# Kernel tuning notes

Measured on AMD Instinct MI355X. Metric: run time of the kernel, lower is better.

Reference implementation:

```python
import jax, jax.numpy as jnp
import numpy as np


def gru_cell(x, h, Wih, Whh, bih, bhh):
    # torch GRU cell, gate order r, z, n
    gi = x @ Wih.T + bih
    gh = h @ Whh.T + bhh
    ir, iz, inn = jnp.split(gi, 3, axis=-1)
    hr, hz, hn = jnp.split(gh, 3, axis=-1)
    r = jax.nn.sigmoid(ir + hr)
    z = jax.nn.sigmoid(iz + hz)
    n = jnp.tanh(inn + r * hn)
    return (1.0 - z) * n + z * h


def setup_inputs() -> dict:
    key = jax.random.key(0)
    ks = jax.random.split(key, 24)
    S, T, B, E, H, V = 64, 64, 32, 512, 1024, 32000
    sc_e = 1.0 / np.sqrt(E)
    sc_h = 1.0 / np.sqrt(H)

    def rn(i, shape, sc):
        return jax.random.normal(ks[i], shape, jnp.float32) * sc

    return {
        "src": jax.random.randint(ks[0], (S, B), 0, V),
        "trg": jax.random.randint(ks[1], (T, B), 0, V),
        "emb": rn(2, (V, E), 0.02),
        # encoder forward-direction GRU
        "Wih_f": rn(3, (3 * H, E), sc_e), "Whh_f": rn(4, (3 * H, H), sc_h),
        "bih_f": rn(5, (3 * H,), sc_h), "bhh_f": rn(6, (3 * H,), sc_h),
        # encoder backward-direction GRU
        "Wih_b": rn(7, (3 * H, E), sc_e), "Whh_b": rn(8, (3 * H, H), sc_h),
        "bih_b": rn(9, (3 * H,), sc_h), "bhh_b": rn(10, (3 * H,), sc_h),
        # attention: Linear(2H -> H) and scoring vector v
        "Wa": rn(11, (H, 2 * H), sc_h), "ba": rn(12, (H,), sc_h),
        "v": rn(13, (H,), sc_h),
        # decoder GRU: input is [embedded(E); context(H)]
        "Wih_d": rn(14, (3 * H, E + H), sc_h), "Whh_d": rn(15, (3 * H, H), sc_h),
        "bih_d": rn(16, (3 * H,), sc_h), "bhh_d": rn(17, (3 * H,), sc_h),
        # output head Linear(2H -> V)
        "Wout": rn(18, (V, 2 * H), sc_h), "bout": rn(19, (V,), sc_h),
    }


def reference(src, trg, emb, Wih_f, Whh_f, bih_f, bhh_f, Wih_b, Whh_b, bih_b, bhh_b,
              Wa, ba, v, Wih_d, Whh_d, bih_d, bhh_d, Wout, bout):
    S, B = src.shape
    H = Whh_f.shape[1]

    # ---- encoder: bidirectional GRU, fwd+bwd output halves summed ----
    src_emb = emb[src]  # [S, B, E]
    h0 = jnp.zeros((B, H), src_emb.dtype)

    def step_f(h, x):
        h2 = gru_cell(x, h, Wih_f, Whh_f, bih_f, bhh_f)
        return h2, h2

    def step_b(h, x):
        h2 = gru_cell(x, h, Wih_b, Whh_b, bih_b, bhh_b)
        return h2, h2

    h_fwd, out_f = jax.lax.scan(step_f, h0, src_emb)
    _, out_b_rev = jax.lax.scan(step_b, h0, src_emb[::-1])
    enc_out = out_f + out_b_rev[::-1]          # [S, B, H]
    enc_bt = enc_out.transpose(1, 0, 2)        # [B, S, H]

    # ---- decoder with teacher forcing (ratio fixed to 1.0) ----
    dec_tokens = jnp.concatenate([src[-1:], trg[:-1]], axis=0)  # [T, B]
    dec_emb = emb[dec_tokens]                                   # [T, B, E]

    def dec_step(h, e_t):
        # Bahdanau attention: relu(Linear([h; enc])) scored by v
        hrep = jnp.broadcast_to(h[:, None, :], enc_bt.shape)    # [B, S, H]
        energy = jax.nn.relu(jnp.concatenate([hrep, enc_bt], -1) @ Wa.T + ba)
        scores = energy @ v                                     # [B, S]
        a = jax.nn.softmax(scores, axis=1)
        ctx = jnp.einsum('bs,bsh->bh', a, enc_bt)               # [B, H]
        rnn_in = jnp.concatenate([e_t, ctx], axis=-1)           # [B, E+H]
        h_new = gru_cell(rnn_in, h, Wih_d, Whh_d, bih_d, bhh_d)
        logits = jnp.concatenate([h_new, ctx], -1) @ Wout.T + bout  # [B, V]
        return h_new, logits

    _, outputs = jax.lax.scan(dec_step, h_fwd, dec_emb)  # [T, B, V]
    return outputs
```

## Files before the change

### kernel.cpp

```cpp
#include <hip/hip_runtime.h>
#include <hip/hip_bf16.h>

#define S_ 64
#define T_ 64
#define B_ 32
#define E_ 512
#define H_ 1024
#define V_ 32000
#define H3 3072
#define H2 2048
#define EH 1536

typedef unsigned short u16;
typedef unsigned int u32;
typedef unsigned long long u64;
typedef __attribute__((ext_vector_type(8))) short bf16x8;
typedef __attribute__((ext_vector_type(4))) float f32x4;

#define MFMA3(ACC, AH_, AL_, BH_, BL_)                                              \
    ACC = __builtin_amdgcn_mfma_f32_16x16x32_bf16(AL_, BH_, ACC, 0, 0, 0);          \
    ACC = __builtin_amdgcn_mfma_f32_16x16x32_bf16(AH_, BL_, ACC, 0, 0, 0);          \
    ACC = __builtin_amdgcn_mfma_f32_16x16x32_bf16(AH_, BH_, ACC, 0, 0, 0);

__device__ __forceinline__ void splitf(float x, u16& h, u16& l) {
    u32 xb = __float_as_uint(x);
    u32 hb = (xb + 0x7FFFu + ((xb >> 16) & 1u)) & 0xFFFF0000u;
    h = (u16)(hb >> 16);
    float lf = x - __uint_as_float(hb);
    u32 lb = __float_as_uint(lf);
    l = (u16)((lb + 0x7FFFu + ((lb >> 16) & 1u)) >> 16);
}

__device__ __forceinline__ float bf2f(u16 v) { return __uint_as_float(((u32)v) << 16); }

__device__ __forceinline__ void load_lds16(const void* g, void* l) {
    __builtin_amdgcn_global_load_lds((const __attribute__((address_space(1))) u32*)g,
                                     (__attribute__((address_space(3))) u32*)l, 16, 0, 0);
}

__device__ __forceinline__ bf16x8 ld_sys16(const u16* p) {
    union { bf16x8 v; u64 q[2]; } u;
    const u64* q = (const u64*)p;
    u.q[0] = __hip_atomic_load(q,     __ATOMIC_RELAXED, __HIP_MEMORY_SCOPE_SYSTEM);
    u.q[1] = __hip_atomic_load(q + 1, __ATOMIC_RELAXED, __HIP_MEMORY_SCOPE_SYSTEM);
    return u.v;
}
__device__ __forceinline__ float ld_sysf(const float* p) {
    return __hip_atomic_load(p, __ATOMIC_RELAXED, __HIP_MEMORY_SCOPE_SYSTEM);
}
__device__ __forceinline__ void st_sysf(float* p, float v) {
    __hip_atomic_store(p, v, __ATOMIC_RELAXED, __HIP_MEMORY_SCOPE_SYSTEM);
}
__device__ __forceinline__ void st_sysu16(u16* p, u16 v) {
    __hip_atomic_store(p, v, __ATOMIC_RELAXED, __HIP_MEMORY_SCOPE_SYSTEM);
}

__device__ __forceinline__ void gbar(int* cnt, int* flag, int nblk, int blk, int& gen) {
    __syncthreads();
    if (threadIdx.x == 0) {
        gen += 1;
        asm volatile("s_waitcnt vmcnt(0)" ::: "memory");
        __hip_atomic_fetch_add(&cnt[(blk & 7) << 5], 1, __ATOMIC_RELAXED,
                               __HIP_MEMORY_SCOPE_SYSTEM);
        if (blk == 0) {
            const int target = nblk * gen;
            for (;;) {
                int sum = 0;
#pragma unroll
                for (int j = 0; j < 8; ++j)
                    sum += __hip_atomic_load(&cnt[j << 5], __ATOMIC_RELAXED,
                                             __HIP_MEMORY_SCOPE_SYSTEM);
                if (sum >= target) break;
                __builtin_amdgcn_s_sleep(2);
            }
#pragma unroll
            for (int j = 0; j < 8; ++j)
                __hip_atomic_store(&flag[j << 5], gen, __ATOMIC_RELAXED,
                                   __HIP_MEMORY_SCOPE_SYSTEM);
        } else {
            while (__hip_atomic_load(&flag[(blk & 7) << 5], __ATOMIC_RELAXED,
                                     __HIP_MEMORY_SCOPE_SYSTEM) < gen)
                __builtin_amdgcn_s_sleep(2);
        }
    }
    __syncthreads();
}

__device__ __forceinline__ void gbar_grp(int* cnt, int grp, int n, int& gen) {
    __syncthreads();
    if (threadIdx.x == 0) {
        gen += 1;
        asm volatile("s_waitcnt vmcnt(0)" ::: "memory");
        __hip_atomic_fetch_add(&cnt[grp << 5], 1, __ATOMIC_RELAXED,
                               __HIP_MEMORY_SCOPE_SYSTEM);
        const int target = n * gen;
        while (__hip_atomic_load(&cnt[grp << 5], __ATOMIC_RELAXED,
                                 __HIP_MEMORY_SCOPE_SYSTEM) < target)
            __builtin_amdgcn_s_sleep(1);
    }
    __syncthreads();
}

__global__ void k_embed_src_split(const int* __restrict__ src, const float* __restrict__ emb,
                                  u16* __restrict__ hi, u16* __restrict__ lo) {
    int row = blockIdx.x;
    int tok = src[row];
    int c = threadIdx.x * 4;
    float4 v = *reinterpret_cast<const float4*>(emb + (size_t)tok * E_ + c);
    ushort4 h, l;
    splitf(v.x, h.x, l.x); splitf(v.y, h.y, l.y);
    splitf(v.z, h.z, l.z); splitf(v.w, h.w, l.w);
    *reinterpret_cast<ushort4*>(hi + (size_t)row * E_ + c) = h;
    *reinterpret_cast<ushort4*>(lo + (size_t)row * E_ + c) = l;
}

__global__ void k_embed_dec_split(const int* __restrict__ src, const int* __restrict__ trg,
                                  const float* __restrict__ emb,
                                  u16* __restrict__ hi, u16* __restrict__ lo) {
    int row = blockIdx.x;
    int t = row >> 5, b = row & 31;
    int tok = (t == 0) ? src[(S_ - 1) * B_ + b] : trg[(t - 1) * B_ + b];
    int c = threadIdx.x * 4;
    float4 v = *reinterpret_cast<const float4*>(emb + (size_t)tok * E_ + c);
    ushort4 h, l;
    splitf(v.x, h.x, l.x); splitf(v.y, h.y, l.y);
    splitf(v.z, h.z, l.z); splitf(v.w, h.w, l.w);
    *reinterpret_cast<ushort4*>(hi + (size_t)row * E_ + c) = h;
    *reinterpret_cast<ushort4*>(lo + (size_t)row * E_ + c) = l;
}

__global__ __launch_bounds__(256) void k_split(const float* __restrict__ in, int ld, int cols4,
                                               u16* __restrict__ hi, u16* __restrict__ lo) {
    int c4 = blockIdx.x * 256 + threadIdx.x;
    if (c4 >= cols4) return;
    size_t r = blockIdx.y;
    float4 v = *reinterpret_cast<const float4*>(in + r * ld + (size_t)c4 * 4);
    ushort4 h, l;
    splitf(v.x, h.x, l.x); splitf(v.y, h.y, l.y);
    splitf(v.z, h.z, l.z); splitf(v.w, h.w, l.w);
    size_t o = (r * cols4 + c4) * 4;
    *reinterpret_cast<ushort4*>(hi + o) = h;
    *reinterpret_cast<ushort4*>(lo + o) = l;
}

__global__ __launch_bounds__(256) void k_split_sum_enc(
    const float* __restrict__ ef, const float* __restrict__ eb, float* __restrict__ es,
    u16* __restrict__ hi, u16* __restrict__ lo) {
    size_t r = blockIdx.y;
    int c4 = threadIdx.x * 4;
    float4 va = *reinterpret_cast<const float4*>(ef + r * H_ + c4);
    float4 vb = *reinterpret_cast<const float4*>(eb + r * H_ + c4);
    float4 v; v.x = va.x + vb.x; v.y = va.y + vb.y; v.z = va.z + vb.z; v.w = va.w + vb.w;
    *reinterpret_cast<float4*>(es + r * H_ + c4) = v;
    ushort4 h, l;
    splitf(v.x, h.x, l.x); splitf(v.y, h.y, l.y);
    splitf(v.z, h.z, l.z); splitf(v.w, h.w, l.w);
    *reinterpret_cast<ushort4*>(hi + r * H_ + c4) = h;
    *reinterpret_cast<ushort4*>(lo + r * H_ + c4) = l;
}

__global__ void k_wsplit_perm(const float* __restrict__ src, int ld, int coff,
                              u16* __restrict__ hi, u16* __restrict__ lo) {
    int r = blockIdx.x;
    int i = r / 3, g = r - i * 3;
    const float* p = src + (size_t)(g * H_ + i) * ld + coff;
    int c = threadIdx.x * 4;
    float4 v = *reinterpret_cast<const float4*>(p + c);
    ushort4 h, l;
    splitf(v.x, h.x, l.x); splitf(v.y, h.y, l.y);
    splitf(v.z, h.z, l.z); splitf(v.w, h.w, l.w);
    *reinterpret_cast<ushort4*>(hi + (size_t)r * H_ + c) = h;
    *reinterpret_cast<ushort4*>(lo + (size_t)r * H_ + c) = l;
}

__global__ __launch_bounds__(256, 2) void k_gemm_mfma3(
    const u16* __restrict__ Ah, const u16* __restrict__ Al,
    const u16* __restrict__ Bh, const u16* __restrict__ Bl,
    const float* __restrict__ bias, float* __restrict__ C,
    int ldc, int K)
{
    __shared__ u16 ls[4][128 * 32];
    const int tid = threadIdx.x;
    const int lane = tid & 63, w = tid >> 6;
    const int wr = w >> 1, wc = w & 1;
    const size_t m0 = (size_t)blockIdx.x * 128, n0 = (size_t)blockIdx.y * 128;

    const int c0 = (w * 2) * 64 + lane;
    const int r0 = c0 >> 2, kc0 = (c0 & 3) << 3;
    const size_t rstep = (size_t)16 * K;
    const u16* gAh = Ah + (m0 + r0) * K + kc0;
    const u16* gAl = Al + (m0 + r0) * K + kc0;
    const u16* gBh = Bh + (n0 + r0) * K + kc0;
    const u16* gBl = Bl + (n0 + r0) * K + kc0;
    const int lo0 = c0 * 8;

    const int frow = lane & 15, fk = (lane >> 4) << 3;
    const int offA = (wr * 64 + frow) * 32 + fk;
    const int offB = (wc * 64 + frow) * 32 + fk;

    f32x4 acc[4][4] = {};

    for (int k0 = 0; k0 < K; k0 += 32) {
        load_lds16(gAh + k0, &ls[0][lo0]);
        load_lds16(gAh + rstep + k0, &ls[0][lo0 + 512]);
        load_lds16(gAl + k0, &ls[1][lo0]);
        load_lds16(gAl + rstep + k0, &ls[1][lo0 + 512]);
        load_lds16(gBh + k0, &ls[2][lo0]);
        load_lds16(gBh + rstep + k0, &ls[2][lo0 + 512]);
        load_lds16(gBl + k0, &ls[3][lo0]);
        load_lds16(gBl + rstep + k0, &ls[3][lo0 + 512]);
        __syncthreads();

        bf16x8 fAh[4], fAl[4], fBh[4], fBl[4];
#pragma unroll
        for (int m = 0; m < 4; ++m) {
            fAh[m] = *reinterpret_cast<const bf16x8*>(&ls[0][offA + m * 512]);
            fAl[m] = *reinterpret_cast<const bf16x8*>(&ls[1][offA + m * 512]);
        }
#pragma unroll
        for (int n = 0; n < 4; ++n) {
            fBh[n] = *reinterpret_cast<const bf16x8*>(&ls[2][offB + n * 512]);
            fBl[n] = *reinterpret_cast<const bf16x8*>(&ls[3][offB + n * 512]);
        }
#pragma unroll
        for (int m = 0; m < 4; ++m)
#pragma unroll
            for (int n = 0; n < 4; ++n) {
                MFMA3(acc[m][n], fAh[m], fAl[m], fBh[n], fBl[n]);
            }
        __syncthreads();
    }

    const int crow0 = wr * 64 + ((lane >> 4) << 2);
    const int ccol0 = wc * 64 + (lane & 15);
#pragma unroll
    for (int n = 0; n < 4; ++n) {
        const size_t col = n0 + ccol0 + n * 16;
        const float bv = bias ? bias[col] : 0.f;
#pragma unroll
        for (int m = 0; m < 4; ++m)
#pragma unroll
            for (int r = 0; r < 4; ++r)
                C[(m0 + crow0 + m * 16 + r) * (size_t)ldc + col] = acc[m][n][r] + bv;
    }
}

__global__ __launch_bounds__(256, 2) void k_gemm_n2f(
    const u16* __restrict__ Ah, const u16* __restrict__ Al,
    const float* __restrict__ Bf,
    const float* __restrict__ bias, float* __restrict__ C,
    int ldc, int K)
{
    __shared__ u16 lsA[2][128 * 32];
    __shared__ u16 lsBh[256 * 32];
    __shared__ u16 lsBl[256 * 32];
    const int tid = threadIdx.x;
    const int lane = tid & 63, w = tid >> 6;
    const int wr = w >> 1, wc = w & 1;
    const size_t m0 = (size_t)blockIdx.x * 128, n0 = (size_t)blockIdx.y * 256;

    const int frow = lane & 15, fk = (lane >> 4) << 3;
    const int offA = (wr * 64 + frow) * 32 + fk;
    const int offB = (wc * 128 + frow) * 32 + fk;

    f32x4 acc[4][8] = {};

    for (int k0 = 0; k0 < K; k0 += 32) {
#pragma unroll
        for (int q = 0; q < 4; ++q) {
            const int chunk = (w + q * 4) * 64 + lane;
            const int local = chunk & 511;
            const u16* A = (chunk < 512) ? Ah : Al;
            load_lds16(A + (m0 + (local >> 2)) * K + k0 + ((local & 3) << 3),
                       &lsA[chunk >> 9][local * 8]);
        }
#pragma unroll
        for (int q = 0; q < 4; ++q) {
            const int c = tid + q * 256;
            const int row = c >> 2, k8 = (c & 3) << 3;
            const float* src = Bf + (size_t)(n0 + row) * K + k0 + k8;
            float4 v0 = *reinterpret_cast<const float4*>(src);
            float4 v1 = *reinterpret_cast<const float4*>(src + 4);
            union { ushort4 s[2]; bf16x8 v; } hh, ll;
            splitf(v0.x, hh.s[0].x, ll.s[0].x); splitf(v0.y, hh.s[0].y, ll.s[0].y);
            splitf(v0.z, hh.s[0].z, ll.s[0].z); splitf(v0.w, hh.s[0].w, ll.s[0].w);
            splitf(v1.x, hh.s[1].x, ll.s[1].x); splitf(v1.y, hh.s[1].y, ll.s[1].y);
            splitf(v1.z, hh.s[1].z, ll.s[1].z); splitf(v1.w, hh.s[1].w, ll.s[1].w);
            *reinterpret_cast<bf16x8*>(&lsBh[row * 32 + k8]) = hh.v;
            *reinterpret_cast<bf16x8*>(&lsBl[row * 32 + k8]) = ll.v;
        }
        __syncthreads();

        bf16x8 fAh[4], fAl[4];
#pragma unroll
        for (int m = 0; m < 4; ++m) {
            fAh[m] = *reinterpret_cast<const bf16x8*>(&lsA[0][offA + m * 512]);
            fAl[m] = *reinterpret_cast<const bf16x8*>(&lsA[1][offA + m * 512]);
        }
#pragma unroll
        for (int n = 0; n < 8; ++n) {
            bf16x8 fBh = *reinterpret_cast<const bf16x8*>(&lsBh[offB + n * 512]);
            bf16x8 fBl = *reinterpret_cast<const bf16x8*>(&lsBl[offB + n * 512]);
#pragma unroll
            for (int m = 0; m < 4; ++m) {
                MFMA3(acc[m][n], fAh[m], fAl[m], fBh, fBl);
            }
        }
        __syncthreads();
    }

    const int crow0 = wr * 64 + ((lane >> 4) << 2);
    const int ccol0 = wc * 128 + (lane & 15);
#pragma unroll
    for (int n = 0; n < 8; ++n) {
        const size_t col = n0 + ccol0 + n * 16;
        const float bv = bias ? bias[col] : 0.f;
#pragma unroll
        for (int m = 0; m < 4; ++m)
#pragma unroll
            for (int r = 0; r < 4; ++r)
                C[(m0 + crow0 + m * 16 + r) * (size_t)ldc + col] = acc[m][n][r] + bv;
    }
}

__global__ __launch_bounds__(256) void k_enc_persist(
    const u16* __restrict__ whhf_h, const u16* __restrict__ whhf_l,
    const u16* __restrict__ whhb_h, const u16* __restrict__ whhb_l,
    const float* __restrict__ gi_f, const float* __restrict__ gi_b,
    const float* __restrict__ bhh_f, const float* __restrict__ bhh_b,
    u16* __restrict__ hfH0, u16* __restrict__ hfL0,
    u16* __restrict__ hfH1, u16* __restrict__ hfL1,
    u16* __restrict__ hbH0, u16* __restrict__ hbL0,
    u16* __restrict__ hbH1, u16* __restrict__ hbL1,
    float* __restrict__ enc_f, float* __restrict__ enc_b,
    int* __restrict__ cnt, int* __restrict__ flag)
{
    __shared__ __align__(16) char smem[145792];
    u16* lAh  = (u16*)smem;
    u16* lAl  = (u16*)(smem + 65536);
    float* ex0 = (float*)(smem + 131072);
    float* ex1 = (float*)(smem + 137408);
    float* hloc = (float*)(smem + 143744);

    const int blk = blockIdx.x, tid = threadIdx.x;
    const int lane = tid & 63, w = tid >> 6;
    const int dir = blk >> 6, c = blk & 63;
    const int i0 = c * 16;
    const u16* WH = (dir ? whhb_h : whhf_h) + (size_t)c * 48 * 1024;
    const u16* WL = (dir ? whhb_l : whhf_l) + (size_t)c * 48 * 1024;
    const float* gi = dir ? gi_b : gi_f;
    const float* bhh = dir ? bhh_b : bhh_f;
    float* encd = dir ? enc_b : enc_f;
    int* cntd  = cnt + dir * 256;
    int* flagd = flag + dir * 256;
    int gen = 0;

    for (int q = tid; q < 512; q += 256) hloc[q] = 0.f;

    const int frow = lane & 15, fk8 = (lane >> 4) << 3;
    const int cb = lane & 15, rb0 = (lane >> 4) << 2;

    for (int t = 0; t < 64; ++t) {
        const int a = t & 1;
        const u16* rH = dir ? (a ? hbH1 : hbH0) : (a ? hfH1 : hfH0);
        const u16* rL = dir ? (a ? hbL1 : hbL0) : (a ? hfL1 : hfL0);
        u16* oH = dir ? (a ? hbH0 : hbH1) : (a ? hfH0 : hfH1);
        u16* oL = dir ? (a ? hbL0 : hbL1) : (a ? hfL0 : hfL1);
        const int s = dir ? 63 - t : t;

#pragma unroll
        for (int ch0 = 0; ch0 < 4096; ch0 += 256) {
            int ch = ch0 + tid;
            int r = ch >> 7, kc = (ch & 127) << 3;
            int sw = kc ^ ((r & 7) << 3);
            *(bf16x8*)&lAh[r * 1024 + sw] = ld_sys16(&rH[r * 1024 + kc]);
            *(bf16x8*)&lAl[r * 1024 + sw] = ld_sys16(&rL[r * 1024 + kc]);
        }
        __syncthreads();

#pragma unroll
        for (int jj = 0; jj < 3; ++jj) {
            const int j = w * 3 + jj;
            const int m = j & 1;
            const int n = (j >> 1) % 3;
            const int kh = j / 6;
            const int arow = m * 16 + frow;
            const int asw = (arow & 7) << 3;
            const u16* gBh = WH + (size_t)(n * 16 + frow) * 1024;
            const u16* gBl = WL + (size_t)(n * 16 + frow) * 1024;
            f32x4 acc = {};
            const int ke = kh * 512 + 512;
#pragma unroll 4
            for (int k0 = kh * 512; k0 < ke; k0 += 32) {
                int kc = k0 + fk8;
                bf16x8 aH = *(const bf16x8*)&lAh[arow * 1024 + (kc ^ asw)];
                bf16x8 aL = *(const bf16x8*)&lAl[arow * 1024 + (kc ^ asw)];
                bf16x8 bH = *(const bf16x8*)&gBh[kc];
                bf16x8 bL = *(const bf16x8*)&gBl[kc];
                MFMA3(acc, aH, aL, bH, bL);
            }
            float* exd = kh ? ex1 : ex0;
            const int pc = n * 16 + cb;
#pragma unroll
            for (int r = 0; r < 4; ++r)
                exd[pc * 33 + m * 16 + rb0 + r] = acc[r];
        }
        __syncthreads();

        {
            const int il = tid & 15, bb = tid >> 4;
            const int i = i0 + il;
#pragma unroll
            for (int q = 0; q < 2; ++q) {
                int b = bb + q * 16;
                float ghr = ex0[(3 * il + 0) * 33 + b] + ex1[(3 * il + 0) * 33 + b] + bhh[i];
                float ghz = ex0[(3 * il + 1) * 33 + b] + ex1[(3 * il + 1) * 33 + b] + bhh[H_ + i];
                float ghn = ex0[(3 * il + 2) * 33 + b] + ex1[(3 * il + 2) * 33 + b] + bhh[2 * H_ + i];
                size_t gio = (size_t)(s * B_ + b) * H3 + i;
                float gir = gi[gio], giz = gi[gio + H_], gin = gi[gio + 2 * H_];
                float rr = 1.f / (1.f + expf(-(gir + ghr)));
                float zz = 1.f / (1.f + expf(-(giz + ghz)));
                float nn = tanhf(gin + rr * ghn);
                float hold = hloc[b * 16 + il];
                float hnew = (1.f - zz) * nn + zz * hold;
                hloc[b * 16 + il] = hnew;
                u16 hh, hl; splitf(hnew, hh, hl);
                st_sysu16(&oH[b * 1024 + i], hh);
                st_sysu16(&oL[b * 1024 + i], hl);
                encd[((size_t)b * 64 + s) * H_ + i] = hnew;
            }
        }
        gbar(cntd, flagd, 64, c, gen);
    }
}

__global__ __launch_bounds__(256) void k_dec_persist(
    const u16* __restrict__ wah, const u16* __restrict__ wal,
    const u16* __restrict__ wgh, const u16* __restrict__ wgl,
    const u16* __restrict__ wdh, const u16* __restrict__ wdl,
    const float* __restrict__ gi_e, const float* __restrict__ bhh_d,
    const float* __restrict__ ep, const float* __restrict__ vvec,
    const float* __restrict__ enc,
    u16* __restrict__ hH, u16* __restrict__ hL,
    float* __restrict__ hwa, float* __restrict__ scores,
    u16* __restrict__ ctxH, u16* __restrict__ ctxL,
    float* __restrict__ states, int* __restrict__ cnt, int* __restrict__ flag,
    int* __restrict__ grpc)
{
    __shared__ __align__(16) char smem[140288];
    u16* lWH  = (u16*)smem;
    u16* lWL  = (u16*)(smem + 32768);
    u16* lDH  = (u16*)(smem + 65536);
    float* lenc = (float*)(smem + 98304);
    float* ex1a = (float*)(smem + 131072);
    float* ex1b = (float*)(smem + 133120);
    float* ex2a = (float*)(smem + 135168);
    float* ex2b = (float*)(smem + 137216);
    float* aw   = (float*)(smem + 139264);
    float* hloc = (float*)(smem + 139520);

    const int bid = blockIdx.x, tid = threadIdx.x;
    const int lane = tid & 63, w = tid >> 6;
    const int frow = lane & 15, fk8 = (lane >> 4) << 3;
    const int b3 = bid >> 3, sl = bid & 7;
    int gen = 0, genG = 0;

    for (int ch = tid; ch < 2048; ch += 256) {
        int r = ch >> 7, kc = (ch & 127) << 3;
        int sw = kc ^ ((r & 7) << 3);
        const u16 *sH, *sL;
        if (r < 4) { sH = wah + ((size_t)bid * 4 + r) * 1024;
                     sL = wal + ((size_t)bid * 4 + r) * 1024; }
        else       { sH = wgh + ((size_t)bid * 12 + r - 4) * 1024;
                     sL = wgl + ((size_t)bid * 12 + r - 4) * 1024; }
        *(bf16x8*)&lWH[r * 1024 + sw] = *(const bf16x8*)&sH[kc];
        *(bf16x8*)&lWL[r * 1024 + sw] = *(const bf16x8*)&sL[kc];
    }
    for (int ch = tid; ch < 2048; ch += 256) {
        int r = ch >> 7, kc = (ch & 127) << 3;
        int sw = kc ^ ((r & 7) << 3);
        int rowg = (r < 12) ? bid * 12 + r : bid * 12;
        *(bf16x8*)&lDH[r * 1024 + sw] = *(const bf16x8*)&wdh[(size_t)rowg * 1024 + kc];
    }
    for (int ch = tid; ch < 2048; ch += 256) {
        int s = ch >> 5, c4 = (ch & 31) << 2;
        *(float4*)&lenc[s * 128 + c4] =
            *(const float4*)&enc[((size_t)b3 * 64 + s) * 1024 + sl * 128 + c4];
    }
    if (tid < 128) {
        int b = tid >> 2, u = bid * 4 + (tid & 3);
        hloc[tid] = bf2f(hH[b * 1024 + u]) + bf2f(hL[b * 1024 + u]);
    }
    float vreg[16];
#pragma unroll
    for (int i = 0; i < 16; ++i) vreg[i] = vvec[lane + i * 64];
    __syncthreads();

    const int mt = w & 1, kh = w >> 1;
    const int bsw = (frow & 7) << 3;
    const int rowg = (frow < 12) ? bid * 12 + frow : bid * 12;
    const u16* gDl = wdl + (size_t)rowg * 1024;
    const int exw = (mt * 16 + ((lane >> 4) << 2)) * 16 + frow;
    const float* epr0 = ep + ((size_t)b3 * 64 + sl * 8 + w * 2) * 1024;
    const float* epr1 = epr0 + 1024;

    for (int t = 0; t < 64; ++t) {
        float pe0[16], pe1[16];
#pragma unroll
        for (int i = 0; i < 16; ++i) pe0[i] = epr0[lane + i * 64];
#pragma unroll
        for (int i = 0; i < 16; ++i) pe1[i] = epr1[lane + i * 64];
        {
            float* exA = kh ? ex1b : ex1a;
            f32x4 acc = {};
            const int ar0 = (mt * 16 + frow) * 1024;
            const int ke = kh * 512 + 512;
#pragma unroll 4
            for (int k0 = kh * 512; k0 < ke; k0 += 32) {
                int kc = k0 + fk8;
                bf16x8 aH = ld_sys16(&hH[ar0 + kc]);
                bf16x8 aL = ld_sys16(&hL[ar0 + kc]);
                bf16x8 bH = *(const bf16x8*)&lWH[frow * 1024 + (kc ^ bsw)];
                bf16x8 bL = *(const bf16x8*)&lWL[frow * 1024 + (kc ^ bsw)];
                MFMA3(acc, aH, aL, bH, bL);
            }
#pragma unroll
            for (int r = 0; r < 4; ++r) exA[exw + r * 16] = acc[r];
        }
        __syncthreads();
        if (tid < 128) {
            int b = tid >> 2, col = tid & 3;
            st_sysf(&hwa[b * 1024 + bid * 4 + col],
                    ex1a[b * 16 + col] + ex1b[b * 16 + col]);
        }
        gbar(cnt, flag, 256, bid, gen);

        {
            float hreg[16];
#pragma unroll
            for (int i = 0; i < 16; ++i)
                hreg[i] = ld_sysf(&hwa[b3 * 1024 + lane + i * 64]);
            float a2 = 0.f, a3 = 0.f;
#pragma unroll
            for (int i = 0; i < 16; ++i) {
                a2 += fmaxf(hreg[i] + pe0[i], 0.f) * vreg[i];
                a3 += fmaxf(hreg[i] + pe1[i], 0.f) * vreg[i];
            }
            for (int off = 32; off; off >>= 1) a2 += __shfl_down(a2, off);
            for (int off = 32; off; off >>= 1) a3 += __shfl_down(a3, off);
            if (lane == 0) {
                st_sysf(&scores[b3 * 64 + sl * 8 + w * 2], a2);
                st_sysf(&scores[b3 * 64 + sl * 8 + w * 2 + 1], a3);
            }
        }
        gbar_grp(grpc, b3, 8, genG);

        if (tid < 64) {
            float sc = ld_sysf(&scores[b3 * 64 + tid]);
            float m = sc;
            for (int off = 32; off; off >>= 1) m = fmaxf(m, __shfl_xor(m, off));
            float e = expf(sc - m);
            float sum = e;
            for (int off = 32; off; off >>= 1) sum += __shfl_xor(sum, off);
            aw[tid] = e / sum;
        }
        __syncthreads();
        if (tid < 128) {
            int c = tid;
            float x = 0.f;
#pragma unroll 8
            for (int s = 0; s < 64; ++s) x += aw[s] * lenc[s * 128 + c];
            states[((size_t)t * 32 + b3) * 2048 + 1024 + sl * 128 + c] = x;
            u16 hh, hl; splitf(x, hh, hl);
            st_sysu16(&ctxH[b3 * 1024 + sl * 128 + c], hh);
            st_sysu16(&ctxL[b3 * 1024 + sl * 128 + c], hl);
        }
        gbar_grp(grpc, b3, 8, genG);

        {
            float* exD = kh ? ex2b : ex2a;
            f32x4 acc = {};
            const int ar0 = (mt * 16 + frow) * 1024;
            const int ke = kh * 512 + 512;
#pragma unroll 4
            for (int k0 = kh * 512; k0 < ke; k0 += 32) {
                int kc = k0 + fk8;
                bf16x8 aH = ld_sys16(&ctxH[ar0 + kc]);
                bf16x8 aL = ld_sys16(&ctxL[ar0 + kc]);
                bf16x8 bH = *(const bf16x8*)&lDH[frow * 1024 + (kc ^ bsw)];
                bf16x8 bL = *(const bf16x8*)&gDl[kc];
                MFMA3(acc, aH, aL, bH, bL);
            }
#pragma unroll
            for (int r = 0; r < 4; ++r) exD[exw + r * 16] = acc[r];
        }
        __syncthreads();
        if (tid < 128) {
            int b = tid >> 2, ui = tid & 3;
            int u = bid * 4 + ui;
            float gicr = ex2a[b * 16 + 3 * ui + 0] + ex2b[b * 16 + 3 * ui + 0];
            float gicz = ex2a[b * 16 + 3 * ui + 1] + ex2b[b * 16 + 3 * ui + 1];
            float gicn = ex2a[b * 16 + 3 * ui + 2] + ex2b[b * 16 + 3 * ui + 2];
            float ghr = ex1a[b * 16 + 4 + 3 * ui + 0] + ex1b[b * 16 + 4 + 3 * ui + 0] + bhh_d[u];
            float ghz = ex1a[b * 16 + 4 + 3 * ui + 1] + ex1b[b * 16 + 4 + 3 * ui + 1] + bhh_d[H_ + u];
            float ghn = ex1a[b * 16 + 4 + 3 * ui + 2] + ex1b[b * 16 + 4 + 3 * ui + 2] + bhh_d[2 * H_ + u];
            size_t ge = ((size_t)t * 32 + b) * 3072;
            float gir = gi_e[ge + u] + gicr;
            float giz = gi_e[ge + 1024 + u] + gicz;
            float gin = gi_e[ge + 2048 + u] + gicn;
            float rr = 1.f / (1.f + expf(-(gir + ghr)));
            float zz = 1.f / (1.f + expf(-(giz + ghz)));
            float nn = tanhf(gin + rr * ghn);
            float hold = hloc[tid];
            float hnew = (1.f - zz) * nn + zz * hold;
            hloc[tid] = hnew;
            u16 hh, hl; splitf(hnew, hh, hl);
            st_sysu16(&hH[b * 1024 + u], hh);
            st_sysu16(&hL[b * 1024 + u], hl);
            states[((size_t)t * 32 + b) * 2048 + u] = hnew;
        }
        gbar(cnt, flag, 256, bid, gen);
    }
}

extern "C" void kernel_launch(void* const* d_in, const int* in_sizes, int n_in,
                              void* d_out, int out_size, void* d_ws, size_t ws_size,
                              hipStream_t stream) {
    const int*   src   = (const int*)d_in[0];
    const int*   trg   = (const int*)d_in[1];
    const float* emb   = (const float*)d_in[2];
    const float* Wih_f = (const float*)d_in[3];
    const float* Whh_f = (const float*)d_in[4];
    const float* bih_f = (const float*)d_in[5];
    const float* bhh_f = (const float*)d_in[6];
    const float* Wih_b = (const float*)d_in[7];
    const float* Whh_b = (const float*)d_in[8];
    const float* bih_b = (const float*)d_in[9];
    const float* bhh_b = (const float*)d_in[10];
    const float* Wa    = (const float*)d_in[11];
    const float* ba    = (const float*)d_in[12];
    const float* vv    = (const float*)d_in[13];
    const float* Wih_d = (const float*)d_in[14];
    const float* Whh_d = (const float*)d_in[15];
    const float* bih_d = (const float*)d_in[16];
    const float* bhh_d = (const float*)d_in[17];
    const float* Wout  = (const float*)d_in[18];
    const float* bout  = (const float*)d_in[19];
    float* out = (float*)d_out;
    (void)in_sizes; (void)n_in; (void)out_size; (void)ws_size;

    float* w = (float*)d_ws;
    size_t o = 0;
    auto alloc = [&](size_t n) { float* p = w + o; o += n; return p; };
    float* gi_f  = alloc((size_t)S_ * B_ * H3);
    float* gi_b  = alloc((size_t)S_ * B_ * H3);
    float* enc_f = alloc((size_t)B_ * S_ * H_);
    float* enc_b = alloc((size_t)B_ * S_ * H_);
    float* enc   = alloc((size_t)B_ * S_ * H_);
    float* ep    = alloc((size_t)B_ * S_ * H_);
    float* hwa   = alloc((size_t)B_ * H_);
    float* scores = alloc(B_ * S_);
    float* barf  = alloc(4096);
    int* cntE  = (int*)barf;
    int* flagE = cntE + 512;
    int* cntD  = cntE + 1024;
    int* flagD = cntE + 1280;
    int* grpD  = cntE + 1536;
    float* gi_e   = gi_f;
    float* states = gi_b;

    u16* wu = (u16*)(w + o);
    size_t ou = 0;
    auto alloc16 = [&](size_t n) { u16* p = wu + ou; ou += n; return p; };
    u16* semb_h  = alloc16((size_t)S_ * B_ * E_);  u16* semb_l  = alloc16((size_t)S_ * B_ * E_);
    u16* demb_h  = alloc16((size_t)T_ * B_ * E_);  u16* demb_l  = alloc16((size_t)T_ * B_ * E_);
    u16* wihf_h  = alloc16((size_t)H3 * E_);       u16* wihf_l  = alloc16((size_t)H3 * E_);
    u16* wihb_h  = alloc16((size_t)H3 * E_);       u16* wihb_l  = alloc16((size_t)H3 * E_);
    u16* wihd_h  = alloc16((size_t)H3 * E_);       u16* wihd_l  = alloc16((size_t)H3 * E_);
    u16* wae_h   = alloc16((size_t)H_ * H_);       u16* wae_l   = alloc16((size_t)H_ * H_);
    u16* enc_h   = alloc16((size_t)B_ * S_ * H_);  u16* enc_l   = alloc16((size_t)B_ * S_ * H_);
    u16* st_h    = alloc16((size_t)T_ * B_ * H2);  u16* st_l    = alloc16((size_t)T_ * B_ * H2);
    u16* whhf_h  = alloc16((size_t)H3 * H_);       u16* whhf_l  = alloc16((size_t)H3 * H_);
    u16* whhb_h  = alloc16((size_t)H3 * H_);       u16* whhb_l  = alloc16((size_t)H3 * H_);
    u16* wgh     = alloc16((size_t)H3 * H_);       u16* wgl     = alloc16((size_t)H3 * H_);
    u16* wdh     = alloc16((size_t)H3 * H_);       u16* wdl     = alloc16((size_t)H3 * H_);
    u16* wah     = alloc16((size_t)H_ * H_);       u16* wal     = alloc16((size_t)H_ * H_);
    u16* hsf_h[2] = {alloc16(B_ * H_), alloc16(B_ * H_)};
    u16* hsf_l[2] = {alloc16(B_ * H_), alloc16(B_ * H_)};
    u16* hsb_h[2] = {alloc16(B_ * H_), alloc16(B_ * H_)};
    u16* hsb_l[2] = {alloc16(B_ * H_), alloc16(B_ * H_)};
    u16* ctx_h   = alloc16(B_ * H_);               u16* ctx_l   = alloc16(B_ * H_);

    hipMemsetAsync(barf, 0, 4096 * sizeof(float), stream);
    hipMemsetAsync(hsf_h[0], 0, B_ * H_ * sizeof(u16), stream);
    hipMemsetAsync(hsf_l[0], 0, B_ * H_ * sizeof(u16), stream);
    hipMemsetAsync(hsb_h[0], 0, B_ * H_ * sizeof(u16), stream);
    hipMemsetAsync(hsb_l[0], 0, B_ * H_ * sizeof(u16), stream);

    k_embed_src_split<<<S_ * B_, 128, 0, stream>>>(src, emb, semb_h, semb_l);
    k_embed_dec_split<<<T_ * B_, 128, 0, stream>>>(src, trg, emb, demb_h, demb_l);

    k_split<<<dim3(1, H3), 256, 0, stream>>>(Wih_f, E_, E_ / 4, wihf_h, wihf_l);
    k_split<<<dim3(1, H3), 256, 0, stream>>>(Wih_b, E_, E_ / 4, wihb_h, wihb_l);
    k_split<<<dim3(1, H3), 256, 0, stream>>>(Wih_d, EH, E_ / 4, wihd_h, wihd_l);
    k_split<<<dim3(1, H_), 256, 0, stream>>>(Wa + H_, H2, H_ / 4, wae_h, wae_l);
    k_split<<<dim3(1, H_), 256, 0, stream>>>(Wa, H2, H_ / 4, wah, wal);
    k_wsplit_perm<<<H3, 256, 0, stream>>>(Whh_f, H_, 0, whhf_h, whhf_l);
    k_wsplit_perm<<<H3, 256, 0, stream>>>(Whh_b, H_, 0, whhb_h, whhb_l);
    k_wsplit_perm<<<H3, 256, 0, stream>>>(Whh_d, H_, 0, wgh, wgl);
    k_wsplit_perm<<<H3, 256, 0, stream>>>(Wih_d, EH, E_, wdh, wdl);

    k_gemm_mfma3<<<dim3(16, 24), 256, 0, stream>>>(semb_h, semb_l, wihf_h, wihf_l,
                                                   bih_f, gi_f, H3, E_);
    k_gemm_mfma3<<<dim3(16, 24), 256, 0, stream>>>(semb_h, semb_l, wihb_h, wihb_l,
                                                   bih_b, gi_b, H3, E_);

    k_enc_persist<<<128, 256, 0, stream>>>(
        whhf_h, whhf_l, whhb_h, whhb_l, gi_f, gi_b, bhh_f, bhh_b,
        hsf_h[0], hsf_l[0], hsf_h[1], hsf_l[1],
        hsb_h[0], hsb_l[0], hsb_h[1], hsb_l[1],
        enc_f, enc_b, cntE, flagE);

    k_split_sum_enc<<<dim3(1, B_ * S_), 256, 0, stream>>>(enc_f, enc_b, enc, enc_h, enc_l);
    k_gemm_mfma3<<<dim3(16, 8), 256, 0, stream>>>(enc_h, enc_l, wae_h, wae_l,
                                                  ba, ep, H_, H_);
    k_gemm_mfma3<<<dim3(16, 24), 256, 0, stream>>>(demb_h, demb_l, wihd_h, wihd_l,
                                                   bih_d, gi_e, H3, E_);

    k_dec_persist<<<256, 256, 0, stream>>>(
        wah, wal, wgh, wgl, wdh, wdl, gi_e, bhh_d, ep, vv, enc,
        hsf_h[0], hsf_l[0], hwa, scores, ctx_h, ctx_l, states, cntD, flagD, grpD);

    k_split<<<dim3(2, T_ * B_), 256, 0, stream>>>(states, H2, H2 / 4, st_h, st_l);
    k_gemm_n2f<<<dim3(16, 125), 256, 0, stream>>>(st_h, st_l, Wout, bout, out, V_, H2);
}
```

Before: 3.998 ms.

## Overlap decoder weight splitting with encoder recurrence and write split states directly

Moves the decoder-side embedding gather and the weight hi/lo splitting kernels into 128 extra blocks of the persistent encoder launch. Those blocks do the work on otherwise idle CUs while the latency-bound recurrence runs. The decoder now writes the bf16 hi/lo state halves directly, which removes the fp32 states buffer and a separate split kernel. The risk is that the extra blocks compete for memory bandwidth with the encoder's barrier-bound steps, or change co-residency of the persistent grid.

```diff
diff --git a/kernel.cpp b/kernel.cpp
--- a/kernel.cpp
+++ b/kernel.cpp
@@ -105,21 +105,6 @@
                                   u16* __restrict__ hi, u16* __restrict__ lo) {
     int row = blockIdx.x;
     int tok = src[row];
-    int c = threadIdx.x * 4;
-    float4 v = *reinterpret_cast<const float4*>(emb + (size_t)tok * E_ + c);
-    ushort4 h, l;
-    splitf(v.x, h.x, l.x); splitf(v.y, h.y, l.y);
-    splitf(v.z, h.z, l.z); splitf(v.w, h.w, l.w);
-    *reinterpret_cast<ushort4*>(hi + (size_t)row * E_ + c) = h;
-    *reinterpret_cast<ushort4*>(lo + (size_t)row * E_ + c) = l;
-}
-
-__global__ void k_embed_dec_split(const int* __restrict__ src, const int* __restrict__ trg,
-                                  const float* __restrict__ emb,
-                                  u16* __restrict__ hi, u16* __restrict__ lo) {
-    int row = blockIdx.x;
-    int t = row >> 5, b = row & 31;
-    int tok = (t == 0) ? src[(S_ - 1) * B_ + b] : trg[(t - 1) * B_ + b];
     int c = threadIdx.x * 4;
     float4 v = *reinterpret_cast<const float4*>(emb + (size_t)tok * E_ + c);
     ushort4 h, l;
@@ -333,7 +318,16 @@
     u16* __restrict__ hbH0, u16* __restrict__ hbL0,
     u16* __restrict__ hbH1, u16* __restrict__ hbL1,
     float* __restrict__ enc_f, float* __restrict__ enc_b,
-    int* __restrict__ cnt, int* __restrict__ flag)
+    int* __restrict__ cnt, int* __restrict__ flag,
+    const int* __restrict__ src, const int* __restrict__ trg,
+    const float* __restrict__ emb, const float* __restrict__ Wih_d,
+    const float* __restrict__ Wa, const float* __restrict__ Whh_d,
+    u16* __restrict__ demb_h, u16* __restrict__ demb_l,
+    u16* __restrict__ wihd_h, u16* __restrict__ wihd_l,
+    u16* __restrict__ wae_h,  u16* __restrict__ wae_l,
+    u16* __restrict__ wahp,   u16* __restrict__ walp,
+    u16* __restrict__ wghp,   u16* __restrict__ wglp,
+    u16* __restrict__ wdhp,   u16* __restrict__ wdlp)
 {
     __shared__ __align__(16) char smem[145792];
     u16* lAh  = (u16*)smem;
@@ -343,6 +337,71 @@
     float* hloc = (float*)(smem + 143744);
 
     const int blk = blockIdx.x, tid = threadIdx.x;
+
+    if (blk >= 128) {
+        const int gt = (blk - 128) * 256 + tid;
+        const int NT = 128 * 256;
+        for (int it = gt; it < 2048 * 128; it += NT) {
+            int row = it >> 7, c = (it & 127) << 2;
+            int tt = row >> 5, b = row & 31;
+            int tok = (tt == 0) ? src[(S_ - 1) * B_ + b] : trg[(tt - 1) * B_ + b];
+            float4 v = *(const float4*)(emb + (size_t)tok * E_ + c);
+            ushort4 h, l;
+            splitf(v.x, h.x, l.x); splitf(v.y, h.y, l.y);
+            splitf(v.z, h.z, l.z); splitf(v.w, h.w, l.w);
+            *(ushort4*)(demb_h + (size_t)row * E_ + c) = h;
+            *(ushort4*)(demb_l + (size_t)row * E_ + c) = l;
+        }
+        for (int it = gt; it < 3072 * 128; it += NT) {
+            int row = it >> 7, c = (it & 127) << 2;
+            float4 v = *(const float4*)(Wih_d + (size_t)row * EH + c);
+            ushort4 h, l;
+            splitf(v.x, h.x, l.x); splitf(v.y, h.y, l.y);
+            splitf(v.z, h.z, l.z); splitf(v.w, h.w, l.w);
+            *(ushort4*)(wihd_h + (size_t)row * E_ + c) = h;
+            *(ushort4*)(wihd_l + (size_t)row * E_ + c) = l;
+        }
+        for (int it = gt; it < 1024 * 256; it += NT) {
+            int row = it >> 8, c = (it & 255) << 2;
+            float4 v = *(const float4*)(Wa + (size_t)row * H2 + H_ + c);
+            ushort4 h, l;
+            splitf(v.x, h.x, l.x); splitf(v.y, h.y, l.y);
+            splitf(v.z, h.z, l.z); splitf(v.w, h.w, l.w);
+            *(ushort4*)(wae_h + (size_t)row * H_ + c) = h;
+            *(ushort4*)(wae_l + (size_t)row * H_ + c) = l;
+        }
+        for (int it = gt; it < 1024 * 256; it += NT) {
+            int row = it >> 8, c = (it & 255) << 2;
+            float4 v = *(const float4*)(Wa + (size_t)row * H2 + c);
+            ushort4 h, l;
+            splitf(v.x, h.x, l.x); splitf(v.y, h.y, l.y);
+            splitf(v.z, h.z, l.z); splitf(v.w, h.w, l.w);
+            *(ushort4*)(wahp + (size_t)row * H_ + c) = h;
+            *(ushort4*)(walp + (size_t)row * H_ + c) = l;
+        }
+        for (int it = gt; it < 3072 * 256; it += NT) {
+            int row = it >> 8, c = (it & 255) << 2;
+            int i = row / 3, g = row - i * 3;
+            float4 v = *(const float4*)(Whh_d + (size_t)(g * H_ + i) * H_ + c);
+            ushort4 h, l;
+            splitf(v.x, h.x, l.x); splitf(v.y, h.y, l.y);
+            splitf(v.z, h.z, l.z); splitf(v.w, h.w, l.w);
+            *(ushort4*)(wghp + (size_t)row * H_ + c) = h;
+            *(ushort4*)(wglp + (size_t)row * H_ + c) = l;
+        }
+        for (int it = gt; it < 3072 * 256; it += NT) {
+            int row = it >> 8, c = (it & 255) << 2;
+            int i = row / 3, g = row - i * 3;
+            float4 v = *(const float4*)(Wih_d + (size_t)(g * H_ + i) * EH + E_ + c);
+            ushort4 h, l;
+            splitf(v.x, h.x, l.x); splitf(v.y, h.y, l.y);
+            splitf(v.z, h.z, l.z); splitf(v.w, h.w, l.w);
+            *(ushort4*)(wdhp + (size_t)row * H_ + c) = h;
+            *(ushort4*)(wdlp + (size_t)row * H_ + c) = l;
+        }
+        return;
+    }
+
     const int lane = tid & 63, w = tid >> 6;
     const int dir = blk >> 6, c = blk & 63;
     const int i0 = c * 16;
@@ -444,8 +503,8 @@
     u16* __restrict__ hH, u16* __restrict__ hL,
     float* __restrict__ hwa, float* __restrict__ scores,
     u16* __restrict__ ctxH, u16* __restrict__ ctxL,
-    float* __restrict__ states, int* __restrict__ cnt, int* __restrict__ flag,
-    int* __restrict__ grpc)
+    u16* __restrict__ st_h, u16* __restrict__ st_l,
+    int* __restrict__ cnt, int* __restrict__ flag, int* __restrict__ grpc)
 {
     __shared__ __align__(16) char smem[140288];
     u16* lWH  = (u16*)smem;
@@ -570,8 +629,9 @@
             float x = 0.f;
 #pragma unroll 8
             for (int s = 0; s < 64; ++s) x += aw[s] * lenc[s * 128 + c];
-            states[((size_t)t * 32 + b3) * 2048 + 1024 + sl * 128 + c] = x;
             u16 hh, hl; splitf(x, hh, hl);
+            size_t so = ((size_t)t * 32 + b3) * 2048 + 1024 + sl * 128 + c;
+            st_h[so] = hh; st_l[so] = hl;
             st_sysu16(&ctxH[b3 * 1024 + sl * 128 + c], hh);
             st_sysu16(&ctxL[b3 * 1024 + sl * 128 + c], hl);
         }
@@ -617,7 +677,8 @@
             u16 hh, hl; splitf(hnew, hh, hl);
             st_sysu16(&hH[b * 1024 + u], hh);
             st_sysu16(&hL[b * 1024 + u], hl);
-            states[((size_t)t * 32 + b) * 2048 + u] = hnew;
+            size_t so = ((size_t)t * 32 + b) * 2048 + u;
+            st_h[so] = hh; st_l[so] = hl;
         }
         gbar(cnt, flag, 256, bid, gen);
     }
@@ -667,7 +728,6 @@
     int* flagD = cntE + 1280;
     int* grpD  = cntE + 1536;
     float* gi_e   = gi_f;
-    float* states = gi_b;
 
     u16* wu = (u16*)(w + o);
     size_t ou = 0;
@@ -698,28 +758,23 @@
     hipMemsetAsync(hsb_l[0], 0, B_ * H_ * sizeof(u16), stream);
 
     k_embed_src_split<<<S_ * B_, 128, 0, stream>>>(src, emb, semb_h, semb_l);
-    k_embed_dec_split<<<T_ * B_, 128, 0, stream>>>(src, trg, emb, demb_h, demb_l);
-
     k_split<<<dim3(1, H3), 256, 0, stream>>>(Wih_f, E_, E_ / 4, wihf_h, wihf_l);
     k_split<<<dim3(1, H3), 256, 0, stream>>>(Wih_b, E_, E_ / 4, wihb_h, wihb_l);
-    k_split<<<dim3(1, H3), 256, 0, stream>>>(Wih_d, EH, E_ / 4, wihd_h, wihd_l);
-    k_split<<<dim3(1, H_), 256, 0, stream>>>(Wa + H_, H2, H_ / 4, wae_h, wae_l);
-    k_split<<<dim3(1, H_), 256, 0, stream>>>(Wa, H2, H_ / 4, wah, wal);
     k_wsplit_perm<<<H3, 256, 0, stream>>>(Whh_f, H_, 0, whhf_h, whhf_l);
     k_wsplit_perm<<<H3, 256, 0, stream>>>(Whh_b, H_, 0, whhb_h, whhb_l);
-    k_wsplit_perm<<<H3, 256, 0, stream>>>(Whh_d, H_, 0, wgh, wgl);
-    k_wsplit_perm<<<H3, 256, 0, stream>>>(Wih_d, EH, E_, wdh, wdl);
-
     k_gemm_mfma3<<<dim3(16, 24), 256, 0, stream>>>(semb_h, semb_l, wihf_h, wihf_l,
                                                    bih_f, gi_f, H3, E_);
     k_gemm_mfma3<<<dim3(16, 24), 256, 0, stream>>>(semb_h, semb_l, wihb_h, wihb_l,
                                                    bih_b, gi_b, H3, E_);
 
-    k_enc_persist<<<128, 256, 0, stream>>>(
+    k_enc_persist<<<256, 256, 0, stream>>>(
         whhf_h, whhf_l, whhb_h, whhb_l, gi_f, gi_b, bhh_f, bhh_b,
         hsf_h[0], hsf_l[0], hsf_h[1], hsf_l[1],
         hsb_h[0], hsb_l[0], hsb_h[1], hsb_l[1],
-        enc_f, enc_b, cntE, flagE);
+        enc_f, enc_b, cntE, flagE,
+        src, trg, emb, Wih_d, Wa, Whh_d,
+        demb_h, demb_l, wihd_h, wihd_l, wae_h, wae_l,
+        wah, wal, wgh, wgl, wdh, wdl);
 
     k_split_sum_enc<<<dim3(1, B_ * S_), 256, 0, stream>>>(enc_f, enc_b, enc, enc_h, enc_l);
     k_gemm_mfma3<<<dim3(16, 8), 256, 0, stream>>>(enc_h, enc_l, wae_h, wae_l,
@@ -729,8 +784,8 @@
 
     k_dec_persist<<<256, 256, 0, stream>>>(
         wah, wal, wgh, wgl, wdh, wdl, gi_e, bhh_d, ep, vv, enc,
-        hsf_h[0], hsf_l[0], hwa, scores, ctx_h, ctx_l, states, cntD, flagD, grpD);
-
-    k_split<<<dim3(2, T_ * B_), 256, 0, stream>>>(states, H2, H2 / 4, st_h, st_l);
+        hsf_h[0], hsf_l[0], hwa, scores, ctx_h, ctx_l, st_h, st_l,
+        cntD, flagD, grpD);
+
     k_gemm_n2f<<<dim3(16, 125), 256, 0, stream>>>(st_h, st_l, Wout, bout, out, V_, H2);
 }
```

Result: no change. 3.997 ms (-0.0%).
